# Kernel optimization log

Measured on AMD Instinct MI355X. Metric: run time of the kernel, lower is better.

Reference implementation:

```python
import jax, jax.numpy as jnp
import numpy as np

LC, LQ, BATCH, D = 1024, 512, 64, 256

def setup_inputs() -> dict:
    key = jax.random.key(0)
    k1, k2, k3, k4, k5 = jax.random.split(key, 5)
    return {
        "C": jax.random.normal(k1, (LC, BATCH, D), dtype=jnp.float32),
        "Q": jax.random.normal(k2, (LQ, BATCH, D), dtype=jnp.float32),
        "w4C": jax.random.normal(k3, (D, 1), dtype=jnp.float32) * 0.05,
        "w4Q": jax.random.normal(k4, (D, 1), dtype=jnp.float32) * 0.05,
        "w4mlu": jax.random.normal(k5, (1, 1, D), dtype=jnp.float32) * 0.05,
        "bias": jnp.zeros((1,), dtype=jnp.float32),
    }

def reference(C, Q, w4C, w4Q, w4mlu, bias):
    # seq-major -> batch-major: (L, B, D) -> (B, L, D)
    C = jnp.transpose(C, (1, 0, 2))  # (B, Lc, D)
    Q = jnp.transpose(Q, (1, 0, 2))  # (B, Lq, D)
    # trilinear attention scores (dropout is identity in eval mode)
    sub0 = C @ w4C                                      # (B, Lc, 1)
    sub1 = jnp.transpose(Q @ w4Q, (0, 2, 1))            # (B, 1, Lq)
    sub2 = jnp.einsum('bcd,bqd->bcq', C * w4mlu, Q)     # (B, Lc, Lq)
    S = sub0 + sub1 + sub2 + bias                       # (B, Lc, Lq)
    S1 = jax.nn.softmax(S, axis=2)   # row softmax over query positions
    S2 = jax.nn.softmax(S, axis=1)   # col softmax over context positions
    A = jnp.einsum('bcq,bqd->bcd', S1, Q)               # (B, Lc, D)
    B_ = jnp.einsum('bck,bqk->bcq', S1, S2)             # S1 @ S2^T : (B, Lc, Lc)
    B_ = jnp.einsum('bce,bed->bcd', B_, C)              # (B, Lc, D)
    out = jnp.concatenate([C, A, C * A, C * B_], axis=2)  # (B, Lc, 4D)
    return jnp.transpose(out, (0, 2, 1))                  # (B, 4D, Lc)
```

## Files before the change

### kernel.cpp

```cpp
#include <hip/hip_runtime.h>

#define LCc 1024
#define LQq 512
#define BB  64
#define DDim 256

typedef __attribute__((ext_vector_type(8))) short bf16x8;
typedef __attribute__((ext_vector_type(4))) float f32x4;
typedef __attribute__((ext_vector_type(4))) unsigned short us4;
typedef __attribute__((ext_vector_type(8))) unsigned short us8;

static __device__ __forceinline__ unsigned short f2b(float f) {
  unsigned u = __builtin_bit_cast(unsigned, f);
  unsigned r = u + 0x7FFFu + ((u >> 16) & 1u);
  return (unsigned short)(r >> 16);
}
static __device__ __forceinline__ bf16x8 ldb8(const unsigned short* p) {
  return *(const bf16x8*)p;
}
static __device__ __forceinline__ f32x4 MFMA16(bf16x8 a, bf16x8 b, f32x4 c) {
  return __builtin_amdgcn_mfma_f32_16x16x32_bf16(a, b, c, 0, 0, 0);
}
static __device__ __forceinline__ void gload16(const unsigned short* g, unsigned short* l) {
  __builtin_amdgcn_global_load_lds(
      (const __attribute__((address_space(1))) unsigned int*)g,
      (__attribute__((address_space(3))) unsigned int*)l, 16, 0, 0);
}

__global__ __launch_bounds__(256, 4) void prep_CF(const float* __restrict__ C,
    const float* __restrict__ w4C, const float* __restrict__ w4mlu,
    unsigned short* __restrict__ Cw, unsigned short* __restrict__ CT,
    float* __restrict__ rowAdd) {
  __shared__ unsigned short tile[64][65];
  int c0 = blockIdx.x * 64, b = blockIdx.y;
  int t = threadIdx.x, r = t >> 2, g = t & 3;
  float rsum = 0.f;
  for (int dch = 0; dch < 4; dch++) {
    int d0 = dch * 64;
    const float* src = C + ((size_t)(c0 + r) * BB + b) * DDim + d0 + g * 16;
    unsigned short cwv[16];
    #pragma unroll
    for (int i = 0; i < 4; i++) {
      float4 v = ((const float4*)src)[i];
      float4 wm = *(const float4*)(w4mlu + d0 + g * 16 + i * 4);
      float4 wc = *(const float4*)(w4C + d0 + g * 16 + i * 4);
      rsum += v.x * wc.x + v.y * wc.y + v.z * wc.z + v.w * wc.w;
      cwv[i * 4 + 0] = f2b(v.x * wm.x);
      cwv[i * 4 + 1] = f2b(v.y * wm.y);
      cwv[i * 4 + 2] = f2b(v.z * wm.z);
      cwv[i * 4 + 3] = f2b(v.w * wm.w);
      tile[r][g * 16 + i * 4 + 0] = f2b(v.x);
      tile[r][g * 16 + i * 4 + 1] = f2b(v.y);
      tile[r][g * 16 + i * 4 + 2] = f2b(v.z);
      tile[r][g * 16 + i * 4 + 3] = f2b(v.w);
    }
    unsigned short* cwp = Cw + ((size_t)((b << 10) + c0 + r)) * DDim + d0 + g * 16;
    *(us8*)cwp = *(us8*)&cwv[0];
    *(us8*)(cwp + 8) = *(us8*)&cwv[8];
    __syncthreads();
    unsigned short* ctp = CT + ((size_t)((b << 8) + d0 + r)) * LCc + c0 + g * 16;
    us8 o0, o1;
    #pragma unroll
    for (int j = 0; j < 8; j++) { o0[j] = tile[g * 16 + j][r]; o1[j] = tile[g * 16 + 8 + j][r]; }
    *(us8*)ctp = o0;
    *(us8*)(ctp + 8) = o1;
    __syncthreads();
  }
  rsum += __shfl_xor(rsum, 1);
  rsum += __shfl_xor(rsum, 2);
  if (g == 0) rowAdd[((size_t)b << 10) + c0 + r] = rsum;
}

__global__ __launch_bounds__(256, 4) void prep_QF(const float* __restrict__ Q,
    const float* __restrict__ w4Q, const float* __restrict__ bias,
    unsigned short* __restrict__ Qb, unsigned short* __restrict__ QT,
    float* __restrict__ colAdd, float* __restrict__ colL) {
  __shared__ unsigned short tile[64][65];
  int q0 = blockIdx.x * 64, b = blockIdx.y;
  int t = threadIdx.x, r = t >> 2, g = t & 3;
  float rsum = 0.f;
  for (int dch = 0; dch < 4; dch++) {
    int d0 = dch * 64;
    const float* src = Q + ((size_t)(q0 + r) * BB + b) * DDim + d0 + g * 16;
    #pragma unroll
    for (int i = 0; i < 4; i++) {
      float4 v = ((const float4*)src)[i];
      float4 wq = *(const float4*)(w4Q + d0 + g * 16 + i * 4);
      rsum += v.x * wq.x + v.y * wq.y + v.z * wq.z + v.w * wq.w;
      tile[r][g * 16 + i * 4 + 0] = f2b(v.x);
      tile[r][g * 16 + i * 4 + 1] = f2b(v.y);
      tile[r][g * 16 + i * 4 + 2] = f2b(v.z);
      tile[r][g * 16 + i * 4 + 3] = f2b(v.w);
    }
    __syncthreads();
    unsigned short* qbp = Qb + ((size_t)((b << 9) + q0 + r)) * DDim + d0 + g * 16;
    us8 s0, s1;
    #pragma unroll
    for (int j = 0; j < 8; j++) { s0[j] = tile[r][g * 16 + j]; s1[j] = tile[r][g * 16 + 8 + j]; }
    *(us8*)qbp = s0;
    *(us8*)(qbp + 8) = s1;
    unsigned short* qtp = QT + ((size_t)((b << 8) + d0 + r)) * LQq + q0 + g * 16;
    us8 o0, o1;
    #pragma unroll
    for (int j = 0; j < 8; j++) { o0[j] = tile[g * 16 + j][r]; o1[j] = tile[g * 16 + 8 + j][r]; }
    *(us8*)qtp = o0;
    *(us8*)(qtp + 8) = o1;
    __syncthreads();
  }
  rsum += __shfl_xor(rsum, 1);
  rsum += __shfl_xor(rsum, 2);
  if (g == 0) {
    colAdd[((size_t)b << 9) + q0 + r] = rsum + bias[0];
    colL[((size_t)b << 9) + q0 + r] = 0.0f;
  }
}

__global__ __launch_bounds__(256, 3) void k_P(const unsigned short* __restrict__ Cw,
    const unsigned short* __restrict__ Qb, const float* __restrict__ rowAdd,
    const float* __restrict__ colAdd, unsigned short* __restrict__ Pt,
    float* __restrict__ rowL, float* __restrict__ colL) {
  int blk = blockIdx.x;
  int b = blk >> 4, ct = blk & 15;
  int t = threadIdx.x, w = t >> 6, lane = t & 63;
  int col = lane & 15, quad = lane >> 4;
  int c0w = ct * 64 + w * 16;
  __shared__ unsigned short tile[2][64][40];
  __shared__ float colAcc[LQq];
  for (int i = t; i < LQq; i += 256) colAcc[i] = 0.f;
  __syncthreads();

  bf16x8 afrag[8];
  const unsigned short* aPtr = Cw + ((size_t)((b << 10) + c0w + col)) * DDim + quad * 8;
  #pragma unroll
  for (int kk = 0; kk < 8; kk++) afrag[kk] = ldb8(aPtr + kk * 32);
  float rAddv[4];
  #pragma unroll
  for (int r = 0; r < 4; r++) rAddv[r] = rowAdd[((size_t)b << 10) + c0w + quad * 4 + r];
  float rowSum[4] = {0.f, 0.f, 0.f, 0.f};

  int cur = 0;
  for (int win = 0; win < 16; win++) {
    #pragma unroll
    for (int h = 0; h < 2; h++) {
      int q0 = win * 32 + h * 16;
      const unsigned short* bPtr = Qb + ((size_t)((b << 9) + q0 + col)) * DDim + quad * 8;
      f32x4 acc = {0.f, 0.f, 0.f, 0.f};
      #pragma unroll
      for (int kk = 0; kk < 8; kk++) acc = MFMA16(afrag[kk], ldb8(bPtr + kk * 32), acc);
      float cAdd = colAdd[((size_t)b << 9) + q0 + col];
      float csum = 0.f;
      #pragma unroll
      for (int r = 0; r < 4; r++) {
        float e = __expf(acc[r] + rAddv[r] + cAdd);
        rowSum[r] += e;
        csum += e;
        tile[cur][w * 16 + quad * 4 + r][h * 16 + col] = f2b(e);
      }
      csum += __shfl_xor(csum, 16);
      csum += __shfl_xor(csum, 32);
      if (lane < 16) atomicAdd(&colAcc[q0 + lane], csum);
    }
    __syncthreads();
    us8 frag = *(const us8*)&tile[cur][w * 16 + col][quad * 8];
    *(us8*)(Pt + (((size_t)(b * 64 + ct * 4 + w) * 16 + win) << 9) + lane * 8) = frag;
    cur ^= 1;
  }
  #pragma unroll
  for (int r = 0; r < 4; r++) {
    float s = rowSum[r];
    s += __shfl_xor(s, 1); s += __shfl_xor(s, 2);
    s += __shfl_xor(s, 4); s += __shfl_xor(s, 8);
    if (col == 0) rowL[((size_t)b << 10) + c0w + quad * 4 + r] = s;
  }
  __syncthreads();
  for (int i = t; i < LQq; i += 256) atomicAdd(&colL[((size_t)b << 9) + i], colAcc[i]);
}

__global__ __launch_bounds__(256, 4) void k_T(const unsigned short* __restrict__ Pt,
    const unsigned short* __restrict__ CT, const float* __restrict__ colL,
    unsigned short* __restrict__ TT) {
  int blk = blockIdx.x;
  int b = blk >> 4, qs = blk & 15;
  int t = threadIdx.x, w = t >> 6, lane = t & 63;
  int col = lane & 15, quad = lane >> 4;
  int dq = w * 64;
  int cbl = w & 1, jh = w >> 1;
  __shared__ unsigned short pT[32][40];

  f32x4 accT[2][4];
  #pragma unroll
  for (int mf = 0; mf < 2; mf++)
    #pragma unroll
    for (int nf = 0; nf < 4; nf++) accT[mf][nf] = (f32x4){0.f, 0.f, 0.f, 0.f};

  us8 frag = *(const us8*)(Pt + (((size_t)(b * 64 + 0 * 2 + cbl) * 16 + qs) << 9) + lane * 8);
  for (int cs = 0; cs < 32; cs++) {
    bf16x8 bf[4];
    #pragma unroll
    for (int nf = 0; nf < 4; nf++)
      bf[nf] = ldb8(CT + ((size_t)((b << 8) + dq + nf * 16 + col)) * LCc + cs * 32 + quad * 8);
    #pragma unroll
    for (int jj = 0; jj < 4; jj++) {
      int j = jh * 4 + jj;
      pT[quad * 8 + j][cbl * 16 + col] = (unsigned short)frag[j];
    }
    __syncthreads();
    bf16x8 pa[2];
    #pragma unroll
    for (int mf = 0; mf < 2; mf++) pa[mf] = *(const bf16x8*)&pT[mf * 16 + col][quad * 8];
    #pragma unroll
    for (int mf = 0; mf < 2; mf++)
      #pragma unroll
      for (int nf = 0; nf < 4; nf++) accT[mf][nf] = MFMA16(pa[mf], bf[nf], accT[mf][nf]);
    if (cs < 31)
      frag = *(const us8*)(Pt + (((size_t)(b * 64 + (cs + 1) * 2 + cbl) * 16 + qs) << 9) + lane * 8);
    __syncthreads();
  }
  float cInv[2][4];
  #pragma unroll
  for (int mf = 0; mf < 2; mf++)
    #pragma unroll
    for (int r = 0; r < 4; r++)
      cInv[mf][r] = 1.0f / colL[((size_t)b << 9) + qs * 32 + mf * 16 + quad * 4 + r];
  #pragma unroll
  for (int mf = 0; mf < 2; mf++)
    #pragma unroll
    for (int nf = 0; nf < 4; nf++) {
      us4 ov;
      #pragma unroll
      for (int r = 0; r < 4; r++) ov[r] = f2b(accT[mf][nf][r] * cInv[mf][r]);
      *(us4*)(TT + ((size_t)((b << 8) + dq + nf * 16 + col)) * LQq + qs * 32 + mf * 16 + quad * 4) = ov;
    }
}

__global__ __launch_bounds__(256, 2) void k_AB(const unsigned short* __restrict__ Pt,
    const unsigned short* __restrict__ QT, const unsigned short* __restrict__ TT,
    const float* __restrict__ rowL, const float* __restrict__ C,
    float* __restrict__ out) {
  int blk = blockIdx.x;
  int b = blk >> 4, ct = blk & 15;
  int t = threadIdx.x, w = t >> 6, lane = t & 63;
  int col = lane & 15, quad = lane >> 4;
  int dq = w * 64;
  __shared__ unsigned short sb[4][2][8][512];

  f32x4 accA[4][4], accB[4][4];
  #pragma unroll
  for (int mf = 0; mf < 4; mf++)
    #pragma unroll
    for (int nf = 0; nf < 4; nf++) {
      accA[mf][nf] = (f32x4){0.f, 0.f, 0.f, 0.f};
      accB[mf][nf] = (f32x4){0.f, 0.f, 0.f, 0.f};
    }

  #define STAGE(qs_, buf_)                                                              \
    {                                                                                   \
      int _q = (qs_) * 32 + quad * 8;                                                   \
      _Pragma("unroll")                                                                 \
      for (int nf = 0; nf < 4; nf++) {                                                  \
        size_t rowD = (size_t)((b << 8) + dq + nf * 16 + col);                          \
        gload16(QT + (rowD << 9) + _q, &sb[w][buf_][nf][0]);                            \
        gload16(TT + (rowD << 9) + _q, &sb[w][buf_][4 + nf][0]);                        \
      }                                                                                 \
    }

  bf16x8 pa[4], paN[4];
  #pragma unroll
  for (int mf = 0; mf < 4; mf++)
    pa[mf] = ldb8(Pt + (((size_t)(b * 64 + ct * 4 + mf) * 16 + 0) << 9) + lane * 8);
  STAGE(0, 0);
  __syncthreads();

  for (int qs = 0; qs < 16; qs++) {
    int bufr = qs & 1;
    if (qs < 15) {
      STAGE(qs + 1, bufr ^ 1);
      #pragma unroll
      for (int mf = 0; mf < 4; mf++)
        paN[mf] = ldb8(Pt + (((size_t)(b * 64 + ct * 4 + mf) * 16 + qs + 1) << 9) + lane * 8);
    }
    bf16x8 bq[4], bt[4];
    #pragma unroll
    for (int nf = 0; nf < 4; nf++) {
      bq[nf] = ldb8(&sb[w][bufr][nf][lane * 8]);
      bt[nf] = ldb8(&sb[w][bufr][4 + nf][lane * 8]);
    }
    #pragma unroll
    for (int mf = 0; mf < 4; mf++)
      #pragma unroll
      for (int nf = 0; nf < 4; nf++) {
        accA[mf][nf] = MFMA16(pa[mf], bq[nf], accA[mf][nf]);
        accB[mf][nf] = MFMA16(pa[mf], bt[nf], accB[mf][nf]);
      }
    if (qs < 15) {
      #pragma unroll
      for (int mf = 0; mf < 4; mf++) pa[mf] = paN[mf];
    }
    __syncthreads();
  }

  float rInv[4][4];
  #pragma unroll
  for (int mf = 0; mf < 4; mf++) {
    float4 rv = *(const float4*)(rowL + ((size_t)b << 10) + ct * 64 + mf * 16 + quad * 4);
    rInv[mf][0] = 1.0f / rv.x; rInv[mf][1] = 1.0f / rv.y;
    rInv[mf][2] = 1.0f / rv.z; rInv[mf][3] = 1.0f / rv.w;
  }
  size_t outB = (size_t)b << 20;
  #pragma unroll
  for (int mf = 0; mf < 4; mf++) {
    int cc = ct * 64 + mf * 16 + quad * 4;
    #pragma unroll
    for (int nf = 0; nf < 4; nf++) {
      int d = dq + nf * 16 + col;
      float4 vC, vA, vCA, vCB;
      #pragma unroll
      for (int r = 0; r < 4; r++) {
        float Cv = C[((size_t)(cc + r) * BB + b) * DDim + d];
        float Av = accA[mf][nf][r] * rInv[mf][r];
        float Bv = accB[mf][nf][r] * rInv[mf][r];
        ((float*)&vC)[r] = Cv;
        ((float*)&vA)[r] = Av;
        ((float*)&vCA)[r] = Cv * Av;
        ((float*)&vCB)[r] = Cv * Bv;
      }
      float* o0 = out + outB + (size_t)d * LCc + cc;
      *(float4*)(o0) = vC;
      *(float4*)(o0 + (size_t)DDim * LCc) = vA;
      *(float4*)(o0 + 2 * (size_t)DDim * LCc) = vCA;
      *(float4*)(o0 + 3 * (size_t)DDim * LCc) = vCB;
    }
  }
  #undef STAGE
}

extern "C" void kernel_launch(void* const* d_in, const int* in_sizes, int n_in,
                              void* d_out, int out_size, void* d_ws, size_t ws_size,
                              hipStream_t stream) {
  const float* C    = (const float*)d_in[0];
  const float* Q    = (const float*)d_in[1];
  const float* w4C  = (const float*)d_in[2];
  const float* w4Q  = (const float*)d_in[3];
  const float* w4mlu= (const float*)d_in[4];
  const float* bias = (const float*)d_in[5];
  float* out = (float*)d_out;
  char* ws = (char*)d_ws;

  unsigned short* Cw = (unsigned short*)(ws);
  unsigned short* CT = (unsigned short*)(ws + 33554432);
  unsigned short* Qb = (unsigned short*)(ws + 67108864);
  unsigned short* TT = Qb;
  unsigned short* QT = (unsigned short*)(ws + 83886080);
  unsigned short* Pt = (unsigned short*)(ws + 100663296);
  float* rowAdd = (float*)(ws + 167772160);
  float* colAdd = (float*)(ws + 168034304);
  float* rowL   = (float*)(ws + 168165376);
  float* colL   = (float*)(ws + 168427520);

  prep_CF<<<dim3(LCc / 64, BB), 256, 0, stream>>>(C, w4C, w4mlu, Cw, CT, rowAdd);
  prep_QF<<<dim3(LQq / 64, BB), 256, 0, stream>>>(Q, w4Q, bias, Qb, QT, colAdd, colL);
  k_P<<<BB * 16, 256, 0, stream>>>(Cw, Qb, rowAdd, colAdd, Pt, rowL, colL);
  k_T<<<BB * 16, 256, 0, stream>>>(Pt, CT, colL, TT);
  k_AB<<<BB * 16, 256, 0, stream>>>(Pt, QT, TT, rowL, C, out);
}
```

Before: 687.3 us.

## Deepen prefetch of P tiles and replace block barriers with explicit vmcnt waits

```diff
diff --git a/kernel.cpp b/kernel.cpp
--- a/kernel.cpp
+++ b/kernel.cpp
@@ -263,40 +263,48 @@
         gload16(TT + (rowD << 9) + _q, &sb[w][buf_][4 + nf][0]);                        \
       }                                                                                 \
     }
-
-  bf16x8 pa[4], paN[4];
-  #pragma unroll
-  for (int mf = 0; mf < 4; mf++)
-    pa[mf] = ldb8(Pt + (((size_t)(b * 64 + ct * 4 + mf) * 16 + 0) << 9) + lane * 8);
+  #define PTLOAD(qs_, set_)                                                             \
+    {                                                                                   \
+      _Pragma("unroll")                                                                 \
+      for (int mf = 0; mf < 4; mf++)                                                    \
+        pa[set_][mf] = ldb8(ptB + mf * 8192 + (qs_) * 512);                             \
+    }
+  #define SBAR __builtin_amdgcn_sched_barrier(0)
+
+  const unsigned short* ptB = Pt + (((size_t)(b * 64 + ct * 4) * 16) << 9) + lane * 8;
+  bf16x8 pa[3][4];
+
+  SBAR;
   STAGE(0, 0);
-  __syncthreads();
-
+  SBAR;
+  PTLOAD(0, 0);
+  SBAR;
+  PTLOAD(1, 1);
+  SBAR;
+
+  #pragma unroll
   for (int qs = 0; qs < 16; qs++) {
-    int bufr = qs & 1;
-    if (qs < 15) {
-      STAGE(qs + 1, bufr ^ 1);
-      #pragma unroll
-      for (int mf = 0; mf < 4; mf++)
-        paN[mf] = ldb8(Pt + (((size_t)(b * 64 + ct * 4 + mf) * 16 + qs + 1) << 9) + lane * 8);
-    }
+    if (qs < 15) { STAGE(qs + 1, (qs + 1) & 1); }
+    SBAR;
+    if (qs < 14) { PTLOAD(qs + 2, (qs + 2) % 3); }
+    SBAR;
+    if (qs < 14)      asm volatile("s_waitcnt vmcnt(16)" ::: "memory");
+    else if (qs == 14) asm volatile("s_waitcnt vmcnt(12)" ::: "memory");
+    else               asm volatile("s_waitcnt vmcnt(0)" ::: "memory");
+    SBAR;
     bf16x8 bq[4], bt[4];
     #pragma unroll
     for (int nf = 0; nf < 4; nf++) {
-      bq[nf] = ldb8(&sb[w][bufr][nf][lane * 8]);
-      bt[nf] = ldb8(&sb[w][bufr][4 + nf][lane * 8]);
+      bq[nf] = ldb8(&sb[w][qs & 1][nf][lane * 8]);
+      bt[nf] = ldb8(&sb[w][qs & 1][4 + nf][lane * 8]);
     }
     #pragma unroll
     for (int mf = 0; mf < 4; mf++)
       #pragma unroll
       for (int nf = 0; nf < 4; nf++) {
-        accA[mf][nf] = MFMA16(pa[mf], bq[nf], accA[mf][nf]);
-        accB[mf][nf] = MFMA16(pa[mf], bt[nf], accB[mf][nf]);
+        accA[mf][nf] = MFMA16(pa[qs % 3][mf], bq[nf], accA[mf][nf]);
+        accB[mf][nf] = MFMA16(pa[qs % 3][mf], bt[nf], accB[mf][nf]);
       }
-    if (qs < 15) {
-      #pragma unroll
-      for (int mf = 0; mf < 4; mf++) pa[mf] = paN[mf];
-    }
-    __syncthreads();
   }
 
   float rInv[4][4];
@@ -332,6 +340,8 @@
     }
   }
   #undef STAGE
+  #undef PTLOAD
+  #undef SBAR
 }
 
 extern "C" void kernel_launch(void* const* d_in, const int* in_sizes, int n_in,
```

New measurement: 699.8 us. About the same (+1.8%).
